# Kernel optimization log

Measured on AMD Instinct MI355X. Metric: run time of the kernel, lower is better.

Reference implementation:

```python
import jax, jax.numpy as jnp
import numpy as np

EMBED_DIM = 1024
NUM_HEADS = 16
NUM_KV_HEADS = 4
HEAD_DIM = 64
WINDOW_SIZE = 32
TOKENS_PER_FRAME = 64
BASE_T, BASE_D, BASE_B = 10000.0, 100.0, 100.0


def apply_3d_rope(x, pos_t, pos_d, pos_b):
    # x: (B, S, H, D); pos_*: (S,) int
    D = x.shape[-1]
    half = D // 2
    dim_idx = jnp.arange(half, dtype=jnp.float32)
    inv_freq = 1.0 / (BASE_T ** (2.0 * dim_idx / D))  # (half,)
    ang = (pos_t.astype(jnp.float32)[:, None] * inv_freq
           + pos_d.astype(jnp.float32)[:, None] * inv_freq * (BASE_T / BASE_D)
           + pos_b.astype(jnp.float32)[:, None] * inv_freq * (BASE_T / BASE_B))  # (S, half)
    cos = jnp.cos(ang)[None, :, None, :]
    sin = jnp.sin(ang)[None, :, None, :]
    x1 = x[..., 0::2]
    x2 = x[..., 1::2]
    y1 = x1 * cos - x2 * sin
    y2 = x1 * sin + x2 * cos
    return jnp.stack([y1, y2], axis=-1).reshape(x.shape)


def setup_inputs() -> dict:
    key = jax.random.key(0)
    ks = jax.random.split(key, 8)
    B, Sn, Lp = 1, 1024, 4096
    hidden_states = jax.random.normal(ks[0], (B, Sn, EMBED_DIM), dtype=jnp.float32)
    past_k = jax.random.normal(ks[1], (B, NUM_KV_HEADS, Lp, HEAD_DIM), dtype=jnp.float32)
    past_v = jax.random.normal(ks[2], (B, NUM_KV_HEADS, Lp, HEAD_DIM), dtype=jnp.float32)
    wq = jax.random.normal(ks[3], (EMBED_DIM, NUM_HEADS * HEAD_DIM), dtype=jnp.float32) * 0.02
    wk = jax.random.normal(ks[4], (EMBED_DIM, NUM_KV_HEADS * HEAD_DIM), dtype=jnp.float32) * 0.02
    wv = jax.random.normal(ks[5], (EMBED_DIM, NUM_KV_HEADS * HEAD_DIM), dtype=jnp.float32) * 0.02
    wo = jax.random.normal(ks[6], (NUM_HEADS * HEAD_DIM, EMBED_DIM), dtype=jnp.float32) * 0.02
    # frame-time positions: tokens_per_frame tokens share a frame time; past frames 0..63, new frames 64..79
    past_idx = jnp.arange(Lp, dtype=jnp.int32)
    new_idx = jnp.arange(Sn, dtype=jnp.int32)
    past_t = past_idx // TOKENS_PER_FRAME
    new_t = new_idx // TOKENS_PER_FRAME + Lp // TOKENS_PER_FRAME
    # 8x8 depth-by-bearing patch grid within each frame
    past_d = (past_idx % TOKENS_PER_FRAME) // 8
    past_b = past_idx % 8
    new_d = (new_idx % TOKENS_PER_FRAME) // 8
    new_b = new_idx % 8
    return dict(hidden_states=hidden_states, past_k=past_k, past_v=past_v,
                wq=wq, wk=wk, wv=wv, wo=wo,
                new_t=new_t, new_d=new_d, new_b=new_b,
                past_t=past_t, past_d=past_d, past_b=past_b)


def reference(hidden_states, past_k, past_v, wq, wk, wv, wo,
              new_t, new_d, new_b, past_t, past_d, past_b):
    B, Sn, _ = hidden_states.shape
    Lp = past_t.shape[0]
    Q = (hidden_states @ wq).reshape(B, Sn, NUM_HEADS, HEAD_DIM)
    Kn = (hidden_states @ wk).reshape(B, Sn, NUM_KV_HEADS, HEAD_DIM)
    Vn = (hidden_states @ wv).reshape(B, Sn, NUM_KV_HEADS, HEAD_DIM)
    Q = apply_3d_rope(Q, new_t, new_d, new_b)
    Kn = apply_3d_rope(Kn, new_t, new_d, new_b)
    Q = Q.transpose(0, 2, 1, 3)   # (B, H, Sn, D)
    Kn = Kn.transpose(0, 2, 1, 3)  # (B, KVH, Sn, D)
    Vn = Vn.transpose(0, 2, 1, 3)
    # Sliding-window truncation on frame time: torch does searchsorted + slice
    # (drop past keys with time < min_time). Masking those keys to -inf is
    # mathematically identical and jit-friendly (static shapes).
    min_time = new_t.max() - (WINDOW_SIZE - 1)
    past_keep = past_t >= min_time                                    # (Lp,)
    valid = jnp.concatenate([past_keep, jnp.ones((Sn,), dtype=bool)])  # (Lp+Sn,)
    pos_t = jnp.concatenate([past_t, new_t])
    K = jnp.concatenate([past_k, Kn], axis=2)  # (B, KVH, Lp+Sn, D)
    V = jnp.concatenate([past_v, Vn], axis=2)
    rep = NUM_HEADS // NUM_KV_HEADS
    K = jnp.repeat(K, rep, axis=1)  # (B, H, L, D) -- repeat_interleave semantics
    V = jnp.repeat(V, rep, axis=1)
    scores = jnp.einsum('bhqd,bhkd->bhqk', Q, K) / jnp.sqrt(jnp.float32(HEAD_DIM))
    mask = (pos_t[None, :] <= new_t[:, None]) & valid[None, :]  # (Sn, L) frame-causal + window
    scores = jnp.where(mask[None, None], scores, jnp.float32(-jnp.inf))
    attn = jax.nn.softmax(scores, axis=-1)
    attn = jnp.nan_to_num(attn)  # fully-masked rows -> 0 (matches torch nan_to_num)
    out = jnp.einsum('bhqk,bhkd->bhqd', attn, V)
    out = out.transpose(0, 2, 1, 3).reshape(B, Sn, NUM_HEADS * HEAD_DIM)
    out = out @ wo
    return out, Kn, Vn
```

## Files before the change

kernel.cpp:

```cpp
#include <hip/hip_runtime.h>
#include <math.h>

#define EMBED 1024
#define NH 16
#define NKV 4
#define HD 64
#define SN 1024
#define LP 4096
#define WIN 32

#define FREQ_C 0.4152410118609203f

typedef float floatx4 __attribute__((ext_vector_type(4)));
typedef __bf16 bf16x8 __attribute__((ext_vector_type(8)));

__global__ __launch_bounds__(256) void qkv_mfma_kernel(
    const float* __restrict__ hidden, const float* __restrict__ wq,
    const float* __restrict__ wk, const float* __restrict__ wv,
    float* __restrict__ pqkv)
{
    __shared__ __bf16 ASh[64][40];
    __shared__ __bf16 BSh[64][40];

    const int tid = threadIdx.x;
    const int lane = tid & 63, w = tid >> 6;
    const int g = lane >> 4, c = lane & 15;
    const int bx = blockIdx.x, by = blockIdx.y, bz = blockIdx.z;

    int ldb, cbase;
    const float* W;
    if (bx < 16)      { W = wq; ldb = 1024; cbase = bx * 64; }
    else if (bx < 20) { W = wk; ldb = 256;  cbase = (bx - 16) * 64; }
    else              { W = wv; ldb = 256;  cbase = (bx - 20) * 64; }

    const int koff = bz * 512;
    const int arow = tid >> 2, ak = (tid & 3) * 8;
    const float* Ap = hidden + (size_t)(by * 64 + arow) * EMBED + koff + ak;
    const int bn = tid & 63, bk0 = (tid >> 6) * 8;
    const float* Bp = W + (size_t)(koff + bk0) * ldb + cbase + bn;

    floatx4 acc[4] = {floatx4(0.f), floatx4(0.f), floatx4(0.f), floatx4(0.f)};

    float a0[8], b0[8];
    *(float4*)&a0[0] = *(const float4*)(Ap);
    *(float4*)&a0[4] = *(const float4*)(Ap + 4);
#pragma unroll
    for (int j = 0; j < 8; j++) b0[j] = Bp[(size_t)j * ldb];

    const int strip = w * 16;

    for (int k0 = 0; k0 < 512; k0 += 32) {
        __syncthreads();
        {
            bf16x8 av, bv;
#pragma unroll
            for (int j = 0; j < 8; j++) { av[j] = (__bf16)a0[j]; bv[j] = (__bf16)b0[j]; }
            *(bf16x8*)&ASh[arow][ak] = av;
            *(bf16x8*)&BSh[bn][bk0] = bv;
        }
        __syncthreads();
        if (k0 + 32 < 512) {
            *(float4*)&a0[0] = *(const float4*)(Ap + k0 + 32);
            *(float4*)&a0[4] = *(const float4*)(Ap + k0 + 36);
#pragma unroll
            for (int j = 0; j < 8; j++) b0[j] = Bp[(size_t)(k0 + 32 + j) * ldb];
        }
        bf16x8 af = *(const bf16x8*)&ASh[strip + c][g * 8];
#pragma unroll
        for (int t = 0; t < 4; t++) {
            bf16x8 bf = *(const bf16x8*)&BSh[t * 16 + c][g * 8];
            acc[t] = __builtin_amdgcn_mfma_f32_16x16x32_bf16(af, bf, acc[t], 0, 0, 0);
        }
    }

    const int m0 = strip + g * 4;
    float* dst = pqkv + (size_t)bz * SN * 1536;
#pragma unroll
    for (int r = 0; r < 4; r++) {
        const int token = by * 64 + m0 + r;
#pragma unroll
        for (int t = 0; t < 4; t++)
            dst[(size_t)token * 1536 + bx * 64 + t * 16 + c] = acc[t][r];
    }
}

__global__ __launch_bounds__(384) void qkv_rope_merge_kernel(
    const float* __restrict__ pqkv, const int* __restrict__ new_t,
    const int* __restrict__ new_d, const int* __restrict__ new_b,
    float* __restrict__ qws, float* __restrict__ knp, float* __restrict__ vnp)
{
    const int row = blockIdx.x;
    const int col = threadIdx.x * 4;
    const float* a = pqkv + (size_t)row * 1536 + col;
    const float* b = a + (size_t)SN * 1536;
    float4 x = *(const float4*)a;
    float4 y = *(const float4*)b;
    float v0 = x.x + y.x, v1 = x.y + y.y, v2 = x.z + y.z, v3 = x.w + y.w;

    if (col < 1280) {
        const int d = col & 63;
        const float j0 = (float)(d >> 1);
        const float f0 = exp2f(-FREQ_C * j0);
        const float f1 = exp2f(-FREQ_C * (j0 + 1.0f));
        const float ft = (float)new_t[row];
        const float fdb = (float)(new_d[row] + new_b[row]);
        float s0, c0, s1, c1;
        sincosf(ft * f0 + fdb * (f0 * 100.0f), &s0, &c0);
        sincosf(ft * f1 + fdb * (f1 * 100.0f), &s1, &c1);
        const float r0 = v0 * c0 - v1 * s0;
        const float r1 = v0 * s0 + v1 * c0;
        const float r2 = v2 * c1 - v3 * s1;
        const float r3 = v2 * s1 + v3 * c1;
        if (col < 1024) {
            *(float4*)&qws[(size_t)row * EMBED + col] = make_float4(r0, r1, r2, r3);
        } else {
            const int kvh = (col - 1024) >> 6;
            *(float4*)&knp[((size_t)kvh * SN + row) * HD + d] = make_float4(r0, r1, r2, r3);
        }
    } else {
        const int kvh = (col - 1280) >> 6;
        *(float4*)&vnp[((size_t)kvh * SN + row) * HD + (col & 63)] =
            make_float4(v0, v1, v2, v3);
    }
}

__global__ __launch_bounds__(256) void out_mfma_kernel(
    const float* __restrict__ A, const float* __restrict__ W,
    float* __restrict__ outp)
{
    __shared__ __bf16 ASh[64][40];
    __shared__ __bf16 BSh[64][40];

    const int tid = threadIdx.x;
    const int lane = tid & 63, w = tid >> 6;
    const int g = lane >> 4, c = lane & 15;
    const int bx = blockIdx.x, by = blockIdx.y, bz = blockIdx.z;

    const int koff = bz * 512;
    const int arow = tid >> 2, ak = (tid & 3) * 8;
    const float* Ap = A + (size_t)(by * 64 + arow) * EMBED + koff + ak;
    const int bn = tid & 63, bk0 = (tid >> 6) * 8;
    const float* Bp = W + (size_t)(koff + bk0) * EMBED + bx * 64 + bn;

    floatx4 acc[4] = {floatx4(0.f), floatx4(0.f), floatx4(0.f), floatx4(0.f)};

    float a0[8], b0[8];
    *(float4*)&a0[0] = *(const float4*)(Ap);
    *(float4*)&a0[4] = *(const float4*)(Ap + 4);
#pragma unroll
    for (int j = 0; j < 8; j++) b0[j] = Bp[(size_t)j * EMBED];

    const int strip = w * 16;

    for (int k0 = 0; k0 < 512; k0 += 32) {
        __syncthreads();
        {
            bf16x8 av, bv;
#pragma unroll
            for (int j = 0; j < 8; j++) { av[j] = (__bf16)a0[j]; bv[j] = (__bf16)b0[j]; }
            *(bf16x8*)&ASh[arow][ak] = av;
            *(bf16x8*)&BSh[bn][bk0] = bv;
        }
        __syncthreads();
        if (k0 + 32 < 512) {
            *(float4*)&a0[0] = *(const float4*)(Ap + k0 + 32);
            *(float4*)&a0[4] = *(const float4*)(Ap + k0 + 36);
#pragma unroll
            for (int j = 0; j < 8; j++) b0[j] = Bp[(size_t)(k0 + 32 + j) * EMBED];
        }
        bf16x8 af = *(const bf16x8*)&ASh[strip + c][g * 8];
#pragma unroll
        for (int t = 0; t < 4; t++) {
            bf16x8 bf = *(const bf16x8*)&BSh[t * 16 + c][g * 8];
            acc[t] = __builtin_amdgcn_mfma_f32_16x16x32_bf16(af, bf, acc[t], 0, 0, 0);
        }
    }

    const int m0 = strip + g * 4;
    float* dst = outp + (size_t)bz * SN * EMBED;
#pragma unroll
    for (int r = 0; r < 4; r++) {
        const int row = by * 64 + m0 + r;
#pragma unroll
        for (int t = 0; t < 4; t++)
            dst[(size_t)row * EMBED + bx * 64 + t * 16 + c] = acc[t][r];
    }
}

__global__ __launch_bounds__(256) void out_merge_kernel(
    const float* __restrict__ outp, float* __restrict__ out)
{
    const size_t i = ((size_t)blockIdx.x * 256 + threadIdx.x) * 4;
    float4 x = *(const float4*)(outp + i);
    float4 y = *(const float4*)(outp + (size_t)SN * EMBED + i);
    *(float4*)(out + i) = make_float4(x.x + y.x, x.y + y.y, x.z + y.z, x.w + y.w);
}


#define PREFETCH_CHUNK(CI)                                                     \
    {                                                                          \
        const int base_ = (myStart + (CI)) << 6;                               \
        const int gk_ = base_ + skk;                                           \
        if (gk_ < Nk) {                                                        \
            const float* kp_ = (gk_ < nPast)                                   \
                ? past_k + ((size_t)(kvh * LP + p0 + gk_)) * HD + sd0          \
                : knp + ((size_t)(kvh * SN + (gk_ - nPast))) * HD + sd0;       \
            kb0 = *(const float4*)(kp_ + 0);                                   \
            kb1 = *(const float4*)(kp_ + 4);                                   \
            kb2 = *(const float4*)(kp_ + 8);                                   \
            kb3 = *(const float4*)(kp_ + 12);                                  \
        } else {                                                               \
            kb0 = kb1 = kb2 = kb3 = make_float4(0.f, 0.f, 0.f, 0.f);           \
        }                                                                      \
        const int gv0_ = base_ + 2 * kp2;                                      \
        if (gv0_ < Nk) {                                                       \
            const float* vp_ = (gv0_ < nPast)                                  \
                ? past_v + ((size_t)(kvh * LP + p0 + gv0_)) * HD + vdb         \
                : vnp + ((size_t)(kvh * SN + (gv0_ - nPast))) * HD + vdb;      \
            vb00 = *(const float4*)(vp_ + 0);                                  \
            vb01 = *(const float4*)(vp_ + 4);                                  \
        } else {                                                               \
            vb00 = vb01 = make_float4(0.f, 0.f, 0.f, 0.f);                     \
        }                                                                      \
        const int gv1_ = gv0_ + 1;                                             \
        if (gv1_ < Nk) {                                                       \
            const float* vp_ = (gv1_ < nPast)                                  \
                ? past_v + ((size_t)(kvh * LP + p0 + gv1_)) * HD + vdb         \
                : vnp + ((size_t)(kvh * SN + (gv1_ - nPast))) * HD + vdb;      \
            vb10 = *(const float4*)(vp_ + 0);                                  \
            vb11 = *(const float4*)(vp_ + 4);                                  \
        } else {                                                               \
            vb10 = vb11 = make_float4(0.f, 0.f, 0.f, 0.f);                     \
        }                                                                      \
        if (tid < 64) {                                                        \
            const int g2_ = base_ + tid;                                       \
            ptreg = (g2_ < Nk)                                                 \
                ? ((g2_ < nPast) ? past_t[p0 + g2_] : new_t[g2_ - nPast])      \
                : 0x7fffffff;                                                  \
        }                                                                      \
    }

__global__ __launch_bounds__(256) void attn_kernel(
    const float* __restrict__ qws, const float* __restrict__ past_k,
    const float* __restrict__ past_v, const float* __restrict__ knp,
    const float* __restrict__ vnp, const int* __restrict__ new_t,
    const int* __restrict__ past_t, float* __restrict__ opart,
    float* __restrict__ lpart)
{
    __shared__ __bf16 KS[64][72];
    __shared__ __bf16 VS[64][72];
    __shared__ __bf16 PS[64][72];
    __shared__ float MSK[64];

    const int tid = threadIdx.x;
    const int f = blockIdx.x, h = blockIdx.y, sidx = blockIdx.z;
    const int kvh = h >> 2;
    const int lane = tid & 63, w = tid >> 6;
    const int g = lane >> 4, c = lane & 15;

    const int tmax = new_t[SN - 1];
    const int min_time = tmax - (WIN - 1);
    const int qtf = new_t[f * 64];

    int lo = 0, hi = LP;
    while (lo < hi) {
        int mid = (lo + hi) >> 1;
        if (past_t[mid] >= min_time) hi = mid; else lo = mid + 1;
    }
    const int p0 = lo;
    const int nPast = LP - p0;
    const int Nk = nPast + (f + 1) * 64;

    const int nch = (Nk + 63) >> 6;
    const int qch = nch >> 2, rem = nch & 3;
    const int myCount = qch + (sidx < rem ? 1 : 0);
    const int myStart = sidx * qch + (sidx < rem ? sidx : rem);

    bf16x8 aQ[2];
    {
        const int q = f * 64 + w * 16 + c;
        const float* qp = qws + (size_t)q * EMBED + h * HD + g * 8;
#pragma unroll
        for (int s = 0; s < 2; s++) {
            float4 q0 = *(const float4*)(qp + s * 32);
            float4 q1 = *(const float4*)(qp + s * 32 + 4);
            bf16x8 a;
            a[0] = (__bf16)q0.x; a[1] = (__bf16)q0.y;
            a[2] = (__bf16)q0.z; a[3] = (__bf16)q0.w;
            a[4] = (__bf16)q1.x; a[5] = (__bf16)q1.y;
            a[6] = (__bf16)q1.z; a[7] = (__bf16)q1.w;
            aQ[s] = a;
        }
    }

    floatx4 oacc[4] = {floatx4(0.f), floatx4(0.f), floatx4(0.f), floatx4(0.f)};
    floatx4 lacc = floatx4(0.f);
    bf16x8 bOnes;
#pragma unroll
    for (int j = 0; j < 8; j++) bOnes[j] = (__bf16)1.0f;

    const float scale = 0.125f;

    const int skk = tid >> 2, sd0 = (tid & 3) * 16;
    const int kp2 = tid & 31, vdb = (tid >> 5) * 8;

    float4 kb0, kb1, kb2, kb3;
    float4 vb00, vb01, vb10, vb11;
    int ptreg = 0x7fffffff;

    if (myCount > 0) PREFETCH_CHUNK(0);

    for (int chi = 0; chi < myCount; ++chi) {
        __syncthreads();

        {
            bf16x8 t0, t1;
            t0[0] = (__bf16)kb0.x; t0[1] = (__bf16)kb0.y;
            t0[2] = (__bf16)kb0.z; t0[3] = (__bf16)kb0.w;
            t0[4] = (__bf16)kb1.x; t0[5] = (__bf16)kb1.y;
            t0[6] = (__bf16)kb1.z; t0[7] = (__bf16)kb1.w;
            t1[0] = (__bf16)kb2.x; t1[1] = (__bf16)kb2.y;
            t1[2] = (__bf16)kb2.z; t1[3] = (__bf16)kb2.w;
            t1[4] = (__bf16)kb3.x; t1[5] = (__bf16)kb3.y;
            t1[6] = (__bf16)kb3.z; t1[7] = (__bf16)kb3.w;
            *(bf16x8*)&KS[skk][sd0] = t0;
            *(bf16x8*)&KS[skk][sd0 + 8] = t1;
        }
        {
            float e0[8] = {vb00.x, vb00.y, vb00.z, vb00.w,
                           vb01.x, vb01.y, vb01.z, vb01.w};
            float e1[8] = {vb10.x, vb10.y, vb10.z, vb10.w,
                           vb11.x, vb11.y, vb11.z, vb11.w};
#pragma unroll
            for (int j = 0; j < 8; j++) {
                union { __bf16 b[2]; unsigned u; } pk;
                pk.b[0] = (__bf16)e0[j];
                pk.b[1] = (__bf16)e1[j];
                *(unsigned*)&VS[vdb + j][2 * kp2] = pk.u;
            }
        }
        if (tid < 64) {
            const int g2 = ((myStart + chi) << 6) + tid;
            const bool ok = (ptreg <= qtf) && ((g2 >= nPast) || (ptreg >= min_time));
            MSK[tid] = ok ? 0.f : -1e30f;
        }
        __syncthreads();

        if (chi + 1 < myCount) PREFETCH_CHUNK(chi + 1);

        floatx4 sacc[4];
#pragma unroll
        for (int t = 0; t < 4; t++) {
            sacc[t] = floatx4(0.f);
#pragma unroll
            for (int s = 0; s < 2; s++) {
                bf16x8 b = *(const bf16x8*)&KS[t * 16 + c][s * 32 + g * 8];
                sacc[t] = __builtin_amdgcn_mfma_f32_16x16x32_bf16(aQ[s], b, sacc[t], 0, 0, 0);
            }
        }

#pragma unroll
        for (int r = 0; r < 4; r++)
#pragma unroll
            for (int t = 0; t < 4; t++)
                PS[w * 16 + g * 4 + r][t * 16 + c] =
                    (__bf16)__expf(sacc[t][r] * scale + MSK[t * 16 + c]);

#pragma unroll
        for (int s = 0; s < 2; s++) {
            bf16x8 a = *(const bf16x8*)&PS[w * 16 + c][s * 32 + g * 8];
            lacc = __builtin_amdgcn_mfma_f32_16x16x32_bf16(a, bOnes, lacc, 0, 0, 0);
#pragma unroll
            for (int t = 0; t < 4; t++) {
                bf16x8 b = *(const bf16x8*)&VS[t * 16 + c][s * 32 + g * 8];
                oacc[t] = __builtin_amdgcn_mfma_f32_16x16x32_bf16(a, b, oacc[t], 0, 0, 0);
            }
        }
    }

    float* Op = opart + ((size_t)(f * 16 + h) * 4 + sidx) * 4096;
    float* lp = lpart + ((size_t)(f * 16 + h) * 4 + sidx) * 64;
#pragma unroll
    for (int r = 0; r < 4; r++) {
        const int q = w * 16 + g * 4 + r;
#pragma unroll
        for (int t = 0; t < 4; t++)
            Op[(size_t)q * 64 + t * 16 + c] = oacc[t][r];
        if (c == 0) lp[q] = lacc[r];
    }
}

__global__ __launch_bounds__(256) void attn_merge_kernel(
    const float* __restrict__ opart, const float* __restrict__ lpart,
    float* __restrict__ ctx)
{
    const int f = blockIdx.x, h = blockIdx.y;
    const int tid = threadIdx.x;
    const int q = tid >> 2, d0 = (tid & 3) * 16;
    const size_t fh = (size_t)(f * 16 + h);

    float l = 0.f;
#pragma unroll
    for (int s = 0; s < 4; s++) l += lpart[(fh * 4 + s) * 64 + q];
    const float inv = (l > 0.f) ? (1.f / l) : 0.f;

    float o[16] = {};
#pragma unroll
    for (int s = 0; s < 4; s++) {
        const float* Os = opart + (fh * 4 + s) * 4096 + (size_t)q * 64 + d0;
#pragma unroll
        for (int v = 0; v < 4; v++) {
            float4 ov = *(const float4*)(Os + v * 4);
            o[v * 4 + 0] += ov.x;
            o[v * 4 + 1] += ov.y;
            o[v * 4 + 2] += ov.z;
            o[v * 4 + 3] += ov.w;
        }
    }
    float* cp = ctx + (size_t)(f * 64 + q) * EMBED + h * HD + d0;
#pragma unroll
    for (int v = 0; v < 4; v++)
        *(float4*)(cp + v * 4) = make_float4(o[v * 4] * inv, o[v * 4 + 1] * inv,
                                             o[v * 4 + 2] * inv, o[v * 4 + 3] * inv);
}

extern "C" void kernel_launch(void* const* d_in, const int* in_sizes, int n_in,
                              void* d_out, int out_size, void* d_ws, size_t ws_size,
                              hipStream_t stream) {
    const float* hidden = (const float*)d_in[0];
    const float* past_k = (const float*)d_in[1];
    const float* past_v = (const float*)d_in[2];
    const float* wq     = (const float*)d_in[3];
    const float* wk     = (const float*)d_in[4];
    const float* wv     = (const float*)d_in[5];
    const float* wo     = (const float*)d_in[6];
    const int* new_t    = (const int*)d_in[7];
    const int* new_d    = (const int*)d_in[8];
    const int* new_b    = (const int*)d_in[9];
    const int* past_t   = (const int*)d_in[10];

    float* out = (float*)d_out;
    float* knp = out + SN * EMBED;
    float* vnp = knp + NKV * SN * HD;

    float* qws   = (float*)d_ws;
    float* lpart = qws + (size_t)SN * EMBED;
    float* opart = lpart + (size_t)NH * 16 * 4 * 64;
    float* outp  = opart;
    float* pqkv  = opart + (size_t)NH * 16 * 4 * 4096;
    float* ctx   = pqkv;

    qkv_mfma_kernel<<<dim3(24, 16, 2), 256, 0, stream>>>(
        hidden, wq, wk, wv, pqkv);
    qkv_rope_merge_kernel<<<dim3(1024), 384, 0, stream>>>(
        pqkv, new_t, new_d, new_b, qws, knp, vnp);
    attn_kernel<<<dim3(16, 16, 4), 256, 0, stream>>>(
        qws, past_k, past_v, knp, vnp, new_t, past_t, opart, lpart);
    attn_merge_kernel<<<dim3(16, 16), 256, 0, stream>>>(opart, lpart, ctx);
    out_mfma_kernel<<<dim3(16, 16, 2), 256, 0, stream>>>(ctx, wo, outp);
    out_merge_kernel<<<dim3(1024), 256, 0, stream>>>(outp, out);
}
```

Measured before the change: 154.8 us.

## Drop split-K in projection GEMMs and fuse RoPE into QKV epilogue

Both projection GEMMs stop splitting K across two blocks, so each block now runs the full K=1024 loop with a 64-wide K tile per stage. This removes the partial-sum buffers and the separate merge kernels. RoPE is now applied directly in the QKV GEMM epilogue, using lane shuffles to pair even and odd elements. Two fewer kernel launches and much less intermediate global traffic are expected, at the cost of half as many blocks (384 and 256), which lowers parallelism on a large GPU.

```diff
diff --git a/kernel.cpp b/kernel.cpp
--- a/kernel.cpp
+++ b/kernel.cpp
@@ -17,185 +17,185 @@
 __global__ __launch_bounds__(256) void qkv_mfma_kernel(
     const float* __restrict__ hidden, const float* __restrict__ wq,
     const float* __restrict__ wk, const float* __restrict__ wv,
-    float* __restrict__ pqkv)
+    const int* __restrict__ new_t, const int* __restrict__ new_d,
+    const int* __restrict__ new_b,
+    float* __restrict__ qws, float* __restrict__ knp, float* __restrict__ vnp)
 {
-    __shared__ __bf16 ASh[64][40];
-    __shared__ __bf16 BSh[64][40];
+    __shared__ __bf16 ASh[64][72];
+    __shared__ __bf16 BSh[64][72];
 
     const int tid = threadIdx.x;
     const int lane = tid & 63, w = tid >> 6;
     const int g = lane >> 4, c = lane & 15;
-    const int bx = blockIdx.x, by = blockIdx.y, bz = blockIdx.z;
-
-    int ldb, cbase;
+    const int bx = blockIdx.x, by = blockIdx.y;
+
+    int mode, ldb, cbase;
     const float* W;
-    if (bx < 16)      { W = wq; ldb = 1024; cbase = bx * 64; }
-    else if (bx < 20) { W = wk; ldb = 256;  cbase = (bx - 16) * 64; }
-    else              { W = wv; ldb = 256;  cbase = (bx - 20) * 64; }
-
-    const int koff = bz * 512;
-    const int arow = tid >> 2, ak = (tid & 3) * 8;
-    const float* Ap = hidden + (size_t)(by * 64 + arow) * EMBED + koff + ak;
-    const int bn = tid & 63, bk0 = (tid >> 6) * 8;
-    const float* Bp = W + (size_t)(koff + bk0) * ldb + cbase + bn;
+    if (bx < 16)      { mode = 0; W = wq; ldb = 1024; cbase = bx * 64; }
+    else if (bx < 20) { mode = 1; W = wk; ldb = 256;  cbase = (bx - 16) * 64; }
+    else              { mode = 2; W = wv; ldb = 256;  cbase = (bx - 20) * 64; }
+
+    const int arow = tid >> 2, ak = (tid & 3) * 16;
+    const float* Ap = hidden + (size_t)(by * 64 + arow) * EMBED + ak;
+    const int bn = tid & 63, bk0 = (tid >> 6) * 16;
+    const float* Bp = W + (size_t)bk0 * ldb + cbase + bn;
 
     floatx4 acc[4] = {floatx4(0.f), floatx4(0.f), floatx4(0.f), floatx4(0.f)};
 
-    float a0[8], b0[8];
-    *(float4*)&a0[0] = *(const float4*)(Ap);
-    *(float4*)&a0[4] = *(const float4*)(Ap + 4);
-#pragma unroll
-    for (int j = 0; j < 8; j++) b0[j] = Bp[(size_t)j * ldb];
+    float a0[16], b0[16];
+#pragma unroll
+    for (int i = 0; i < 4; i++)
+        *(float4*)&a0[4 * i] = *(const float4*)(Ap + 4 * i);
+#pragma unroll
+    for (int j = 0; j < 16; j++) b0[j] = Bp[(size_t)j * ldb];
 
     const int strip = w * 16;
 
-    for (int k0 = 0; k0 < 512; k0 += 32) {
+    for (int k0 = 0; k0 < EMBED; k0 += 64) {
         __syncthreads();
         {
-            bf16x8 av, bv;
-#pragma unroll
-            for (int j = 0; j < 8; j++) { av[j] = (__bf16)a0[j]; bv[j] = (__bf16)b0[j]; }
-            *(bf16x8*)&ASh[arow][ak] = av;
-            *(bf16x8*)&BSh[bn][bk0] = bv;
-        }
-        __syncthreads();
-        if (k0 + 32 < 512) {
-            *(float4*)&a0[0] = *(const float4*)(Ap + k0 + 32);
-            *(float4*)&a0[4] = *(const float4*)(Ap + k0 + 36);
-#pragma unroll
-            for (int j = 0; j < 8; j++) b0[j] = Bp[(size_t)(k0 + 32 + j) * ldb];
-        }
-        bf16x8 af = *(const bf16x8*)&ASh[strip + c][g * 8];
+            bf16x8 av0, av1, bv0, bv1;
+#pragma unroll
+            for (int j = 0; j < 8; j++) {
+                av0[j] = (__bf16)a0[j];     av1[j] = (__bf16)a0[j + 8];
+                bv0[j] = (__bf16)b0[j];     bv1[j] = (__bf16)b0[j + 8];
+            }
+            *(bf16x8*)&ASh[arow][ak] = av0;
+            *(bf16x8*)&ASh[arow][ak + 8] = av1;
+            *(bf16x8*)&BSh[bn][bk0] = bv0;
+            *(bf16x8*)&BSh[bn][bk0 + 8] = bv1;
+        }
+        __syncthreads();
+        if (k0 + 64 < EMBED) {
+#pragma unroll
+            for (int i = 0; i < 4; i++)
+                *(float4*)&a0[4 * i] = *(const float4*)(Ap + k0 + 64 + 4 * i);
+#pragma unroll
+            for (int j = 0; j < 16; j++) b0[j] = Bp[(size_t)(k0 + 64 + j) * ldb];
+        }
+        bf16x8 af0 = *(const bf16x8*)&ASh[strip + c][g * 8];
+        bf16x8 af1 = *(const bf16x8*)&ASh[strip + c][32 + g * 8];
 #pragma unroll
         for (int t = 0; t < 4; t++) {
-            bf16x8 bf = *(const bf16x8*)&BSh[t * 16 + c][g * 8];
-            acc[t] = __builtin_amdgcn_mfma_f32_16x16x32_bf16(af, bf, acc[t], 0, 0, 0);
+            bf16x8 bf0 = *(const bf16x8*)&BSh[t * 16 + c][g * 8];
+            bf16x8 bf1 = *(const bf16x8*)&BSh[t * 16 + c][32 + g * 8];
+            acc[t] = __builtin_amdgcn_mfma_f32_16x16x32_bf16(af0, bf0, acc[t], 0, 0, 0);
+            acc[t] = __builtin_amdgcn_mfma_f32_16x16x32_bf16(af1, bf1, acc[t], 0, 0, 0);
         }
     }
 
     const int m0 = strip + g * 4;
-    float* dst = pqkv + (size_t)bz * SN * 1536;
-#pragma unroll
-    for (int r = 0; r < 4; r++) {
-        const int token = by * 64 + m0 + r;
-#pragma unroll
-        for (int t = 0; t < 4; t++)
-            dst[(size_t)token * 1536 + bx * 64 + t * 16 + c] = acc[t][r];
-    }
-}
-
-__global__ __launch_bounds__(384) void qkv_rope_merge_kernel(
-    const float* __restrict__ pqkv, const int* __restrict__ new_t,
-    const int* __restrict__ new_d, const int* __restrict__ new_b,
-    float* __restrict__ qws, float* __restrict__ knp, float* __restrict__ vnp)
-{
-    const int row = blockIdx.x;
-    const int col = threadIdx.x * 4;
-    const float* a = pqkv + (size_t)row * 1536 + col;
-    const float* b = a + (size_t)SN * 1536;
-    float4 x = *(const float4*)a;
-    float4 y = *(const float4*)b;
-    float v0 = x.x + y.x, v1 = x.y + y.y, v2 = x.z + y.z, v3 = x.w + y.w;
-
-    if (col < 1280) {
-        const int d = col & 63;
-        const float j0 = (float)(d >> 1);
-        const float f0 = exp2f(-FREQ_C * j0);
-        const float f1 = exp2f(-FREQ_C * (j0 + 1.0f));
-        const float ft = (float)new_t[row];
-        const float fdb = (float)(new_d[row] + new_b[row]);
-        float s0, c0, s1, c1;
-        sincosf(ft * f0 + fdb * (f0 * 100.0f), &s0, &c0);
-        sincosf(ft * f1 + fdb * (f1 * 100.0f), &s1, &c1);
-        const float r0 = v0 * c0 - v1 * s0;
-        const float r1 = v0 * s0 + v1 * c0;
-        const float r2 = v2 * c1 - v3 * s1;
-        const float r3 = v2 * s1 + v3 * c1;
-        if (col < 1024) {
-            *(float4*)&qws[(size_t)row * EMBED + col] = make_float4(r0, r1, r2, r3);
-        } else {
-            const int kvh = (col - 1024) >> 6;
-            *(float4*)&knp[((size_t)kvh * SN + row) * HD + d] = make_float4(r0, r1, r2, r3);
+    if (mode == 2) {
+        const int kvh = bx - 20;
+#pragma unroll
+        for (int r = 0; r < 4; r++) {
+            const int token = by * 64 + m0 + r;
+#pragma unroll
+            for (int t = 0; t < 4; t++)
+                vnp[((size_t)kvh * SN + token) * HD + t * 16 + c] = acc[t][r];
         }
     } else {
-        const int kvh = (col - 1280) >> 6;
-        *(float4*)&vnp[((size_t)kvh * SN + row) * HD + (col & 63)] =
-            make_float4(v0, v1, v2, v3);
+        float fr[4];
+#pragma unroll
+        for (int t = 0; t < 4; t++) {
+            const int d = (cbase + t * 16 + c) & 63;
+            fr[t] = exp2f(-FREQ_C * (float)(d >> 1));
+        }
+        const int par = c & 1;
+#pragma unroll
+        for (int r = 0; r < 4; r++) {
+            const int token = by * 64 + m0 + r;
+            const float ft = (float)new_t[token];
+            const float fdb = (float)(new_d[token] + new_b[token]);
+#pragma unroll
+            for (int t = 0; t < 4; t++) {
+                const float ang = ft * fr[t] + fdb * (fr[t] * 100.0f);
+                float sv, cv;
+                sincosf(ang, &sv, &cv);
+                const float x = acc[t][r];
+                const float xp = __shfl_xor(x, 1, 64);
+                const float y = par ? (xp * sv + x * cv) : (x * cv - xp * sv);
+                if (mode == 0) {
+                    qws[(size_t)token * EMBED + cbase + t * 16 + c] = y;
+                } else {
+                    const int kvh = bx - 16;
+                    knp[((size_t)kvh * SN + token) * HD + t * 16 + c] = y;
+                }
+            }
+        }
     }
 }
 
 __global__ __launch_bounds__(256) void out_mfma_kernel(
     const float* __restrict__ A, const float* __restrict__ W,
-    float* __restrict__ outp)
+    float* __restrict__ C)
 {
-    __shared__ __bf16 ASh[64][40];
-    __shared__ __bf16 BSh[64][40];
+    __shared__ __bf16 ASh[64][72];
+    __shared__ __bf16 BSh[64][72];
 
     const int tid = threadIdx.x;
     const int lane = tid & 63, w = tid >> 6;
     const int g = lane >> 4, c = lane & 15;
-    const int bx = blockIdx.x, by = blockIdx.y, bz = blockIdx.z;
-
-    const int koff = bz * 512;
-    const int arow = tid >> 2, ak = (tid & 3) * 8;
-    const float* Ap = A + (size_t)(by * 64 + arow) * EMBED + koff + ak;
-    const int bn = tid & 63, bk0 = (tid >> 6) * 8;
-    const float* Bp = W + (size_t)(koff + bk0) * EMBED + bx * 64 + bn;
+    const int bx = blockIdx.x, by = blockIdx.y;
+
+    const int arow = tid >> 2, ak = (tid & 3) * 16;
+    const float* Ap = A + (size_t)(by * 64 + arow) * EMBED + ak;
+    const int bn = tid & 63, bk0 = (tid >> 6) * 16;
+    const float* Bp = W + (size_t)bk0 * EMBED + bx * 64 + bn;
 
     floatx4 acc[4] = {floatx4(0.f), floatx4(0.f), floatx4(0.f), floatx4(0.f)};
 
-    float a0[8], b0[8];
-    *(float4*)&a0[0] = *(const float4*)(Ap);
-    *(float4*)&a0[4] = *(const float4*)(Ap + 4);
-#pragma unroll
-    for (int j = 0; j < 8; j++) b0[j] = Bp[(size_t)j * EMBED];
+    float a0[16], b0[16];
+#pragma unroll
+    for (int i = 0; i < 4; i++)
+        *(float4*)&a0[4 * i] = *(const float4*)(Ap + 4 * i);
+#pragma unroll
+    for (int j = 0; j < 16; j++) b0[j] = Bp[(size_t)j * EMBED];
 
     const int strip = w * 16;
 
-    for (int k0 = 0; k0 < 512; k0 += 32) {
+    for (int k0 = 0; k0 < EMBED; k0 += 64) {
         __syncthreads();
         {
-            bf16x8 av, bv;
-#pragma unroll
-            for (int j = 0; j < 8; j++) { av[j] = (__bf16)a0[j]; bv[j] = (__bf16)b0[j]; }
-            *(bf16x8*)&ASh[arow][ak] = av;
-            *(bf16x8*)&BSh[bn][bk0] = bv;
-        }
-        __syncthreads();
-        if (k0 + 32 < 512) {
-            *(float4*)&a0[0] = *(const float4*)(Ap + k0 + 32);
-            *(float4*)&a0[4] = *(const float4*)(Ap + k0 + 36);
-#pragma unroll
-            for (int j = 0; j < 8; j++) b0[j] = Bp[(size_t)(k0 + 32 + j) * EMBED];
-        }
-        bf16x8 af = *(const bf16x8*)&ASh[strip + c][g * 8];
+            bf16x8 av0, av1, bv0, bv1;
+#pragma unroll
+            for (int j = 0; j < 8; j++) {
+                av0[j] = (__bf16)a0[j];     av1[j] = (__bf16)a0[j + 8];
+                bv0[j] = (__bf16)b0[j];     bv1[j] = (__bf16)b0[j + 8];
+            }
+            *(bf16x8*)&ASh[arow][ak] = av0;
+            *(bf16x8*)&ASh[arow][ak + 8] = av1;
+            *(bf16x8*)&BSh[bn][bk0] = bv0;
+            *(bf16x8*)&BSh[bn][bk0 + 8] = bv1;
+        }
+        __syncthreads();
+        if (k0 + 64 < EMBED) {
+#pragma unroll
+            for (int i = 0; i < 4; i++)
+                *(float4*)&a0[4 * i] = *(const float4*)(Ap + k0 + 64 + 4 * i);
+#pragma unroll
+            for (int j = 0; j < 16; j++) b0[j] = Bp[(size_t)(k0 + 64 + j) * EMBED];
+        }
+        bf16x8 af0 = *(const bf16x8*)&ASh[strip + c][g * 8];
+        bf16x8 af1 = *(const bf16x8*)&ASh[strip + c][32 + g * 8];
 #pragma unroll
         for (int t = 0; t < 4; t++) {
-            bf16x8 bf = *(const bf16x8*)&BSh[t * 16 + c][g * 8];
-            acc[t] = __builtin_amdgcn_mfma_f32_16x16x32_bf16(af, bf, acc[t], 0, 0, 0);
+            bf16x8 bf0 = *(const bf16x8*)&BSh[t * 16 + c][g * 8];
+            bf16x8 bf1 = *(const bf16x8*)&BSh[t * 16 + c][32 + g * 8];
+            acc[t] = __builtin_amdgcn_mfma_f32_16x16x32_bf16(af0, bf0, acc[t], 0, 0, 0);
+            acc[t] = __builtin_amdgcn_mfma_f32_16x16x32_bf16(af1, bf1, acc[t], 0, 0, 0);
         }
     }
 
     const int m0 = strip + g * 4;
-    float* dst = outp + (size_t)bz * SN * EMBED;
 #pragma unroll
     for (int r = 0; r < 4; r++) {
         const int row = by * 64 + m0 + r;
 #pragma unroll
         for (int t = 0; t < 4; t++)
-            dst[(size_t)row * EMBED + bx * 64 + t * 16 + c] = acc[t][r];
+            C[(size_t)row * EMBED + bx * 64 + t * 16 + c] = acc[t][r];
     }
 }
-
-__global__ __launch_bounds__(256) void out_merge_kernel(
-    const float* __restrict__ outp, float* __restrict__ out)
-{
-    const size_t i = ((size_t)blockIdx.x * 256 + threadIdx.x) * 4;
-    float4 x = *(const float4*)(outp + i);
-    float4 y = *(const float4*)(outp + (size_t)SN * EMBED + i);
-    *(float4*)(out + i) = make_float4(x.x + y.x, x.y + y.y, x.z + y.z, x.w + y.w);
-}
-
 
 #define PREFETCH_CHUNK(CI)                                                     \
     {                                                                          \
@@ -445,18 +445,13 @@
 
     float* qws   = (float*)d_ws;
     float* lpart = qws + (size_t)SN * EMBED;
-    float* opart = lpart + (size_t)NH * 16 * 4 * 64;
-    float* outp  = opart;
-    float* pqkv  = opart + (size_t)NH * 16 * 4 * 4096;
-    float* ctx   = pqkv;
-
-    qkv_mfma_kernel<<<dim3(24, 16, 2), 256, 0, stream>>>(
-        hidden, wq, wk, wv, pqkv);
-    qkv_rope_merge_kernel<<<dim3(1024), 384, 0, stream>>>(
-        pqkv, new_t, new_d, new_b, qws, knp, vnp);
+    float* opart = lpart + (size_t)16 * 16 * 4 * 64;
+    float* ctx   = opart + (size_t)16 * 16 * 4 * 4096;
+
+    qkv_mfma_kernel<<<dim3(24, 16), 256, 0, stream>>>(
+        hidden, wq, wk, wv, new_t, new_d, new_b, qws, knp, vnp);
     attn_kernel<<<dim3(16, 16, 4), 256, 0, stream>>>(
         qws, past_k, past_v, knp, vnp, new_t, past_t, opart, lpart);
     attn_merge_kernel<<<dim3(16, 16), 256, 0, stream>>>(opart, lpart, ctx);
-    out_mfma_kernel<<<dim3(16, 16, 2), 256, 0, stream>>>(ctx, wo, outp);
-    out_merge_kernel<<<dim3(1024), 256, 0, stream>>>(outp, out);
+    out_mfma_kernel<<<dim3(16, 16), 256, 0, stream>>>(ctx, wo, out);
 }
```

Result: no change. 156.8 us (+1.2%).
